# Kernel tuning notes

Measured on AMD Instinct MI355X. Metric: run time of the kernel, lower is better.

The kernel has to match this reference:

```python
import jax, jax.numpy as jnp
import numpy as np

N_NODES = 500_000
N_EDGES = 16_000_000
N_COLORS = 64


def _mix(v, c1, c2):
    """32-bit integer hash (lowbias32-style avalanche mix)."""
    v = v.astype(jnp.uint32)
    v = (v ^ (v >> 16)) * jnp.uint32(c1)
    v = (v ^ (v >> 13)) * jnp.uint32(c2)
    return v ^ (v >> 16)


def setup_inputs() -> dict:
    key = jax.random.key(0)
    k1, k2 = jax.random.split(key)
    x = jax.random.randint(k1, (N_NODES,), 0, N_COLORS, dtype=jnp.int32)
    edge_index = jax.random.randint(k2, (2, N_EDGES), 0, N_NODES, dtype=jnp.int32)
    return {"x": x, "edge_index": edge_index}


def reference(x, edge_index):
    """One Weisfeiler-Lehman color-refinement step.

    Faithful semantics of WLConvOptimized.forward: each node's new label is
    determined by the equivalence class of (own label, multiset of incoming
    neighbor labels). Instead of Python tuple-sort + hash()+dict, we use a
    permutation-invariant multiset hash (sum of two independent 32-bit hashes
    of neighbor labels, combined with the node's own label hash) and then a
    sort-based dense relabeling. Nodes get equal output labels iff their
    (label, neighbor-multiset) signatures collide -- same partition as the
    original (up to astronomically unlikely hash collisions); label numbering
    is canonical (sorted-signature order) rather than dict-insertion order.
    """
    num_nodes = x.shape[0]
    row, col = edge_index[0], edge_index[1]  # message flows row (src) -> col (dst)

    # two independent per-label hashes
    ha = _mix(x, 0x045D9F3B, 0x045D9F3B)
    hb = _mix(x, 0x9E3779B1, 0x85EBCA77)

    # permutation-invariant multiset hash of incoming neighbor labels (gather + scatter-add)
    sum_a = jnp.zeros(num_nodes, jnp.uint32).at[col].add(ha[row])
    sum_b = jnp.zeros(num_nodes, jnp.uint32).at[col].add(hb[row])

    # combine own label with neighbor multiset, re-avalanche
    sig_a = _mix(ha * jnp.uint32(0x27D4EB2F) + sum_a, 0xC2B2AE3D, 0x165667B1)
    sig_b = _mix(hb * jnp.uint32(0x61C88647) + sum_b, 0x045D9F3B, 0x27D4EB2F)

    # dense relabel: sort by (sig_a, sig_b), number distinct signatures 0..K-1
    order = jnp.lexsort((sig_b, sig_a))
    sa, sb = sig_a[order], sig_b[order]
    new_grp = jnp.concatenate([
        jnp.zeros(1, jnp.int32),
        ((sa[1:] != sa[:-1]) | (sb[1:] != sb[:-1])).astype(jnp.int32),
    ])
    labels_sorted = jnp.cumsum(new_grp).astype(jnp.int32)
    out = jnp.zeros(num_nodes, jnp.int32).at[order].set(labels_sorted)
    return out
```

## Files before the change

kernel.cpp:

```cpp
#include <hip/hip_runtime.h>
#include <stdint.h>

#define LOG_B 17
#define NB (1u << LOG_B)
#define FINE_NODES 1024
#define NBKT 512
#define CSH 10
#define EPB 16384

__host__ __device__ constexpr uint32_t cmix(uint32_t v, uint32_t c1, uint32_t c2) {
    v = (v ^ (v >> 16)) * c1;
    v = (v ^ (v >> 13)) * c2;
    return v ^ (v >> 16);
}

__device__ __forceinline__ uint32_t mixh(uint32_t v, uint32_t c1, uint32_t c2) {
    v = (v ^ (v >> 16)) * c1;
    v = (v ^ (v >> 13)) * c2;
    return v ^ (v >> 16);
}

struct Luts { uint32_t ha[64]; uint32_t hb[64]; };
constexpr Luts make_luts() {
    Luts l{};
    for (uint32_t i = 0; i < 64; i++) {
        l.ha[i] = cmix(i, 0x045D9F3Bu, 0x045D9F3Bu);
        l.hb[i] = cmix(i, 0x9E3779B1u, 0x85EBCA77u);
    }
    return l;
}
__constant__ Luts LUT = make_luts();

__global__ __launch_bounds__(256) void k_pre(const int4* __restrict__ x4,
                                             uchar4* __restrict__ xc4, int n4) {
    int i = blockIdx.x * 256 + threadIdx.x;
    if (i >= n4) return;
    int4 v = x4[i];
    xc4[i] = make_uchar4((uint8_t)v.x, (uint8_t)v.y, (uint8_t)v.z, (uint8_t)v.w);
}

__global__ __launch_bounds__(256) void k_bin(const int* __restrict__ row, const int* __restrict__ col,
                                             const uint8_t* __restrict__ xc, uint16_t* __restrict__ bins,
                                             uint32_t* __restrict__ cursor, int E, int cap) {
    __shared__ uint16_t stage[EPB];
    __shared__ uint32_t hist[NBKT];
    __shared__ uint16_t gb16[NBKT];
    __shared__ uint32_t wsum[4];
    int t = threadIdx.x;
    int lane = t & 63, wid = t >> 6;
    int base = blockIdx.x * EPB;
    int nend = min(E - base, EPB);
    for (int b = t; b < NBKT; b += 256) hist[b] = 0;
    __syncthreads();

    const int4* col4 = (const int4*)(col + base);
    const int4* row4 = (const int4*)(row + base);
    int n4 = nend >> 2;

    for (int k = t; k < n4; k += 256) {
        int4 c = col4[k];
        atomicAdd(&hist[(uint32_t)c.x >> CSH], 1u);
        atomicAdd(&hist[(uint32_t)c.y >> CSH], 1u);
        atomicAdd(&hist[(uint32_t)c.z >> CSH], 1u);
        atomicAdd(&hist[(uint32_t)c.w >> CSH], 1u);
    }
    for (int k = (n4 << 2) + t; k < nend; k += 256)
        atomicAdd(&hist[(uint32_t)col[base + k] >> CSH], 1u);
    __syncthreads();

    int b0 = 2 * t;
    uint32_t h0 = hist[b0], h1 = hist[b0 + 1];
    uint32_t s = h0 + h1;
    uint32_t inc = s;
    for (int off = 1; off < 64; off <<= 1) {
        uint32_t nv = __shfl_up(inc, (unsigned)off, 64);
        if (lane >= off) inc += nv;
    }
    if (lane == 63) wsum[wid] = inc;
    __syncthreads();
    uint32_t woff = 0;
    for (int w = 0; w < wid; w++) woff += wsum[w];
    uint32_t e0 = woff + inc - s;
    uint32_t g0 = h0 ? atomicAdd(&cursor[b0], h0) : 0u;
    uint32_t g1 = h1 ? atomicAdd(&cursor[b0 + 1], h1) : 0u;
    gb16[b0] = (uint16_t)g0;
    gb16[b0 + 1] = (uint16_t)g1;
    hist[b0] = e0 << 16;
    hist[b0 + 1] = (e0 + h0) << 16;
    __syncthreads();

    for (int k = t; k < n4; k += 256) {
        int4 c = col4[k];
        int4 r = row4[k];
        {
            uint32_t d = (uint32_t)c.x, b = d >> CSH;
            uint32_t o = atomicAdd(&hist[b], 1u);
            stage[(o >> 16) + (o & 0xFFFFu)] = (uint16_t)(((d & 1023u) << 6) | (uint32_t)xc[r.x]);
        }
        {
            uint32_t d = (uint32_t)c.y, b = d >> CSH;
            uint32_t o = atomicAdd(&hist[b], 1u);
            stage[(o >> 16) + (o & 0xFFFFu)] = (uint16_t)(((d & 1023u) << 6) | (uint32_t)xc[r.y]);
        }
        {
            uint32_t d = (uint32_t)c.z, b = d >> CSH;
            uint32_t o = atomicAdd(&hist[b], 1u);
            stage[(o >> 16) + (o & 0xFFFFu)] = (uint16_t)(((d & 1023u) << 6) | (uint32_t)xc[r.z]);
        }
        {
            uint32_t d = (uint32_t)c.w, b = d >> CSH;
            uint32_t o = atomicAdd(&hist[b], 1u);
            stage[(o >> 16) + (o & 0xFFFFu)] = (uint16_t)(((d & 1023u) << 6) | (uint32_t)xc[r.w]);
        }
    }
    for (int k = (n4 << 2) + t; k < nend; k += 256) {
        int i = base + k;
        uint32_t d = (uint32_t)col[i], b = d >> CSH;
        uint32_t o = atomicAdd(&hist[b], 1u);
        stage[(o >> 16) + (o & 0xFFFFu)] = (uint16_t)(((d & 1023u) << 6) | (uint32_t)xc[row[i]]);
    }
    __syncthreads();

    int sub = lane >> 4, l16 = lane & 15;
    for (int b = wid * 4 + sub; b < NBKT; b += 16) {
        uint32_t hv = hist[b];
        uint32_t cnt = hv & 0xFFFFu;
        if (!cnt) continue;
        uint32_t s0 = hv >> 16;
        uint16_t* dst = bins + (size_t)b * (uint32_t)cap + gb16[b];
        for (uint32_t off = l16; off < cnt; off += 16)
            dst[off] = stage[s0 + off];
    }
}

__global__ __launch_bounds__(512) void k_accsig(const uint16_t* __restrict__ bins,
                                                const uint32_t* __restrict__ cursor,
                                                const uint8_t* __restrict__ xc,
                                                unsigned long long* __restrict__ sigs,
                                                uint32_t* __restrict__ bcnt, int N, int cap) {
    __shared__ uint32_t cnt[FINE_NODES * 16];
    int t = threadIdx.x;
    int b = blockIdx.x;
    for (int i = t; i < FINE_NODES * 16; i += 512) cnt[i] = 0;
    __syncthreads();
    uint32_t m = cursor[b];
    const uint16_t* mybins = bins + (size_t)b * (uint32_t)cap;
    const uint2* p16v = (const uint2*)mybins;
    uint32_t m4 = m >> 2;
    for (uint32_t k = t; k < m4; k += 512) {
        uint2 rv = p16v[k];
        {
            uint32_t rec = rv.x & 0xFFFFu, n = rec >> 6, c = rec & 63u;
            atomicAdd(&cnt[n * 16 + (c >> 2)], 1u << (8u * (c & 3u)));
        }
        {
            uint32_t rec = rv.x >> 16, n = rec >> 6, c = rec & 63u;
            atomicAdd(&cnt[n * 16 + (c >> 2)], 1u << (8u * (c & 3u)));
        }
        {
            uint32_t rec = rv.y & 0xFFFFu, n = rec >> 6, c = rec & 63u;
            atomicAdd(&cnt[n * 16 + (c >> 2)], 1u << (8u * (c & 3u)));
        }
        {
            uint32_t rec = rv.y >> 16, n = rec >> 6, c = rec & 63u;
            atomicAdd(&cnt[n * 16 + (c >> 2)], 1u << (8u * (c & 3u)));
        }
    }
    for (uint32_t k = (m4 << 2) + t; k < m; k += 512) {
        uint32_t rec = mybins[k], n = rec >> 6, c = rec & 63u;
        atomicAdd(&cnt[n * 16 + (c >> 2)], 1u << (8u * (c & 3u)));
    }
    __syncthreads();

    for (int n = t; n < FINE_NODES; n += 512) {
        int g = b * FINE_NODES + n;
        if (g >= N) break;
        uint32_t sum_a = 0, sum_b = 0;
#pragma unroll
        for (int w = 0; w < 16; w++) {
            uint32_t wp = (uint32_t)(w + n) & 15u;
            uint32_t v = cnt[n * 16 + wp];
            uint32_t c0 = v & 255u, c1 = (v >> 8) & 255u, c2 = (v >> 16) & 255u, c3 = v >> 24;
            sum_a += c0 * LUT.ha[4 * wp] + c1 * LUT.ha[4 * wp + 1]
                   + c2 * LUT.ha[4 * wp + 2] + c3 * LUT.ha[4 * wp + 3];
            sum_b += c0 * LUT.hb[4 * wp] + c1 * LUT.hb[4 * wp + 1]
                   + c2 * LUT.hb[4 * wp + 2] + c3 * LUT.hb[4 * wp + 3];
        }
        uint32_t xv = (uint32_t)xc[g];
        uint32_t ha = LUT.ha[xv];
        uint32_t hb = LUT.hb[xv];
        uint32_t sa = mixh(ha * 0x27D4EB2Fu + sum_a, 0xC2B2AE3Du, 0x165667B1u);
        uint32_t sb = mixh(hb * 0x61C88647u + sum_b, 0x045D9F3Bu, 0x27D4EB2Fu);
        unsigned long long key = ((unsigned long long)sa << 32) | (unsigned long long)sb;
        sigs[g] = key;
        atomicAdd(&bcnt[(uint32_t)(key >> (64 - LOG_B))], 1u);
    }
}

__global__ __launch_bounds__(256) void k_scan1(const uint32_t* __restrict__ in,
                                               uint32_t* __restrict__ out,
                                               uint32_t* __restrict__ part) {
    __shared__ uint32_t wsum[4];
    int t = threadIdx.x;
    int lane = t & 63, wid = t >> 6;
    int base = blockIdx.x * 1024 + 4 * t;
    uint4 v = *(const uint4*)(in + base);
    uint32_t s = v.x + v.y + v.z + v.w;
    uint32_t inc = s;
    for (int off = 1; off < 64; off <<= 1) {
        uint32_t nv = __shfl_up(inc, (unsigned)off, 64);
        if (lane >= off) inc += nv;
    }
    if (lane == 63) wsum[wid] = inc;
    __syncthreads();
    uint32_t woff = 0;
    for (int w = 0; w < wid; w++) woff += wsum[w];
    uint32_t e = woff + inc - s;
    uint4 o;
    o.x = e; o.y = e + v.x; o.z = o.y + v.y; o.w = o.z + v.z;
    *(uint4*)(out + base) = o;
    if (t == 255) part[blockIdx.x] = wsum[0] + wsum[1] + wsum[2] + wsum[3];
}

__global__ void k_scan2(uint32_t* __restrict__ part) {
    __shared__ uint32_t s[256];
    int t = threadIdx.x;
    uint32_t v = part[t];
    s[t] = v;
    __syncthreads();
    for (int off = 1; off < 256; off <<= 1) {
        uint32_t add = (t >= off) ? s[t - off] : 0u;
        __syncthreads();
        s[t] += add;
        __syncthreads();
    }
    part[t] = s[t] - v;
}

__global__ __launch_bounds__(256) void k_scan3(uint32_t* __restrict__ out,
                                               const uint32_t* __restrict__ part) {
    int base = blockIdx.x * 1024 + 4 * threadIdx.x;
    uint32_t p = part[blockIdx.x];
    uint4 v = *(const uint4*)(out + base);
    v.x += p; v.y += p; v.z += p; v.w += p;
    *(uint4*)(out + base) = v;
}

__global__ void k_scatter(const unsigned long long* __restrict__ sigs,
                          const uint32_t* __restrict__ boff, uint32_t* __restrict__ bcur,
                          unsigned long long* __restrict__ skey, uint32_t* __restrict__ snode,
                          int N) {
    int i = blockIdx.x * blockDim.x + threadIdx.x;
    if (i >= N) return;
    unsigned long long key = sigs[i];
    uint32_t b = (uint32_t)(key >> (64 - LOG_B));
    uint32_t pos = boff[b] + atomicAdd(&bcur[b], 1u);
    skey[pos] = key;
    snode[pos] = (uint32_t)i;
}

__global__ void k_bsort(unsigned long long* __restrict__ skey, uint32_t* __restrict__ snode,
                        const uint32_t* __restrict__ boff, uint32_t* __restrict__ ldx,
                        uint32_t* __restrict__ dcnt, int N) {
    int b = blockIdx.x * blockDim.x + threadIdx.x;
    if (b >= (int)NB) return;
    uint32_t s0 = boff[b];
    uint32_t s1 = (b == (int)NB - 1) ? (uint32_t)N : boff[b + 1];
    for (uint32_t i = s0 + 1; i < s1; i++) {
        unsigned long long k = skey[i];
        uint32_t nd = snode[i];
        uint32_t j = i;
        while (j > s0 && skey[j - 1] > k) {
            skey[j] = skey[j - 1];
            snode[j] = snode[j - 1];
            j--;
        }
        skey[j] = k;
        snode[j] = nd;
    }
    uint32_t d = 0;
    unsigned long long prev = 0ull;
    for (uint32_t i = s0; i < s1; i++) {
        unsigned long long k = skey[i];
        if (i == s0 || k != prev) d++;
        prev = k;
        ldx[i] = d - 1;
    }
    dcnt[b] = d;
}

__global__ void k_out(const unsigned long long* __restrict__ skey,
                      const uint32_t* __restrict__ snode, const uint32_t* __restrict__ ldx,
                      const uint32_t* __restrict__ doff, int* __restrict__ out, int N) {
    int i = blockIdx.x * blockDim.x + threadIdx.x;
    if (i >= N) return;
    unsigned long long key = skey[i];
    uint32_t b = (uint32_t)(key >> (64 - LOG_B));
    out[snode[i]] = (int)(doff[b] + ldx[i]);
}

extern "C" void kernel_launch(void* const* d_in, const int* in_sizes, int n_in,
                              void* d_out, int out_size, void* d_ws, size_t ws_size,
                              hipStream_t stream) {
    const int* x = (const int*)d_in[0];
    const int* ei = (const int*)d_in[1];
    int N = in_sizes[0];
    int E = in_sizes[1] / 2;
    const int* row = ei;
    const int* col = ei + E;

    int nacc = (N + FINE_NODES - 1) / FINE_NODES;
    int cap = E / NBKT + (E / NBKT) / 16 + 1024;
    cap = (cap + 3) & ~3;

    char* p = (char*)d_ws;
    auto alloc = [&](size_t bytes) -> char* {
        char* r = p;
        p += (bytes + 255) & ~(size_t)255;
        return r;
    };
    uint32_t* cursor = (uint32_t*)alloc((size_t)NBKT * 4);
    uint32_t* bcnt   = (uint32_t*)alloc((size_t)NB * 4);
    uint32_t* bcur   = (uint32_t*)alloc((size_t)NB * 4);
    uint32_t* dcnt   = (uint32_t*)alloc((size_t)NB * 4);
    uint32_t* part   = (uint32_t*)alloc(256 * 4);
    size_t zbytes = (size_t)(p - (char*)d_ws);
    uint8_t* xc = (uint8_t*)alloc((size_t)N);
    unsigned long long* sigs = (unsigned long long*)alloc((size_t)N * 8);
    uint16_t* bins = (uint16_t*)alloc((size_t)NBKT * cap * 2);
    char* q = (char*)bins;
    auto alias = [&](size_t bytes) -> char* {
        char* r = q;
        q += (bytes + 255) & ~(size_t)255;
        return r;
    };
    unsigned long long* skey = (unsigned long long*)alias((size_t)N * 8);
    uint32_t* snode = (uint32_t*)alias((size_t)N * 4);
    uint32_t* ldx   = (uint32_t*)alias((size_t)N * 4);
    uint32_t* boff  = (uint32_t*)alias((size_t)NB * 4);
    uint32_t* doff  = (uint32_t*)alias((size_t)NB * 4);

    hipMemsetAsync(d_ws, 0, zbytes, stream);

    int nbN = (N + 255) / 256;
    int nbBin = (E + EPB - 1) / EPB;
    int n4 = N / 4;

    k_pre<<<(n4 + 255) / 256, 256, 0, stream>>>((const int4*)x, (uchar4*)xc, n4);
    k_bin<<<nbBin, 256, 0, stream>>>(row, col, xc, bins, cursor, E, cap);
    k_accsig<<<nacc, 512, 0, stream>>>(bins, cursor, xc, sigs, bcnt, N, cap);

    k_scan1<<<NB / 1024, 256, 0, stream>>>(bcnt, boff, part);
    k_scan2<<<1, 256, 0, stream>>>(part);
    k_scan3<<<NB / 1024, 256, 0, stream>>>(boff, part);

    k_scatter<<<nbN, 256, 0, stream>>>(sigs, boff, bcur, skey, snode, N);
    k_bsort<<<NB / 256, 256, 0, stream>>>(skey, snode, boff, ldx, dcnt, N);

    k_scan1<<<NB / 1024, 256, 0, stream>>>(dcnt, doff, part);
    k_scan2<<<1, 256, 0, stream>>>(part);
    k_scan3<<<NB / 1024, 256, 0, stream>>>(doff, part);

    k_out<<<nbN, 256, 0, stream>>>(skey, snode, ldx, doff, (int*)d_out, N);
}
```

Baseline: 434.8 us.

## Replace edge binning and shared-memory histograms with direct global atomic scatter-add

Removes the two-pass bucketed binning of edges and the per-bucket shared-memory color histogram. Each edge now gathers its source label, hashes it inline and does two global atomicAdds into per-node sumA/sumB arrays, followed by a per-node signature kernel. This drops the intermediate bins buffer and one pass over edges, but trades contention-free shared atomics for 32M random global atomics.

```diff
diff --git a/kernel.cpp b/kernel.cpp
--- a/kernel.cpp
+++ b/kernel.cpp
@@ -3,33 +3,12 @@
 
 #define LOG_B 17
 #define NB (1u << LOG_B)
-#define FINE_NODES 1024
-#define NBKT 512
-#define CSH 10
-#define EPB 16384
-
-__host__ __device__ constexpr uint32_t cmix(uint32_t v, uint32_t c1, uint32_t c2) {
-    v = (v ^ (v >> 16)) * c1;
-    v = (v ^ (v >> 13)) * c2;
-    return v ^ (v >> 16);
-}
 
 __device__ __forceinline__ uint32_t mixh(uint32_t v, uint32_t c1, uint32_t c2) {
     v = (v ^ (v >> 16)) * c1;
     v = (v ^ (v >> 13)) * c2;
     return v ^ (v >> 16);
 }
-
-struct Luts { uint32_t ha[64]; uint32_t hb[64]; };
-constexpr Luts make_luts() {
-    Luts l{};
-    for (uint32_t i = 0; i < 64; i++) {
-        l.ha[i] = cmix(i, 0x045D9F3Bu, 0x045D9F3Bu);
-        l.hb[i] = cmix(i, 0x9E3779B1u, 0x85EBCA77u);
-    }
-    return l;
-}
-__constant__ Luts LUT = make_luts();
 
 __global__ __launch_bounds__(256) void k_pre(const int4* __restrict__ x4,
                                              uchar4* __restrict__ xc4, int n4) {
@@ -39,162 +18,58 @@
     xc4[i] = make_uchar4((uint8_t)v.x, (uint8_t)v.y, (uint8_t)v.z, (uint8_t)v.w);
 }
 
-__global__ __launch_bounds__(256) void k_bin(const int* __restrict__ row, const int* __restrict__ col,
-                                             const uint8_t* __restrict__ xc, uint16_t* __restrict__ bins,
-                                             uint32_t* __restrict__ cursor, int E, int cap) {
-    __shared__ uint16_t stage[EPB];
-    __shared__ uint32_t hist[NBKT];
-    __shared__ uint16_t gb16[NBKT];
-    __shared__ uint32_t wsum[4];
-    int t = threadIdx.x;
-    int lane = t & 63, wid = t >> 6;
-    int base = blockIdx.x * EPB;
-    int nend = min(E - base, EPB);
-    for (int b = t; b < NBKT; b += 256) hist[b] = 0;
-    __syncthreads();
-
-    const int4* col4 = (const int4*)(col + base);
-    const int4* row4 = (const int4*)(row + base);
-    int n4 = nend >> 2;
-
-    for (int k = t; k < n4; k += 256) {
+__global__ __launch_bounds__(256) void k_edge(const int4* __restrict__ row4,
+                                              const int4* __restrict__ col4,
+                                              const int* __restrict__ row,
+                                              const int* __restrict__ col,
+                                              const uint8_t* __restrict__ xc,
+                                              uint32_t* __restrict__ sumA,
+                                              uint32_t* __restrict__ sumB,
+                                              int n4, int E) {
+    int stride = gridDim.x * 256;
+    for (int k = blockIdx.x * 256 + threadIdx.x; k < n4; k += stride) {
+        int4 r = row4[k];
         int4 c = col4[k];
-        atomicAdd(&hist[(uint32_t)c.x >> CSH], 1u);
-        atomicAdd(&hist[(uint32_t)c.y >> CSH], 1u);
-        atomicAdd(&hist[(uint32_t)c.z >> CSH], 1u);
-        atomicAdd(&hist[(uint32_t)c.w >> CSH], 1u);
-    }
-    for (int k = (n4 << 2) + t; k < nend; k += 256)
-        atomicAdd(&hist[(uint32_t)col[base + k] >> CSH], 1u);
-    __syncthreads();
-
-    int b0 = 2 * t;
-    uint32_t h0 = hist[b0], h1 = hist[b0 + 1];
-    uint32_t s = h0 + h1;
-    uint32_t inc = s;
-    for (int off = 1; off < 64; off <<= 1) {
-        uint32_t nv = __shfl_up(inc, (unsigned)off, 64);
-        if (lane >= off) inc += nv;
-    }
-    if (lane == 63) wsum[wid] = inc;
-    __syncthreads();
-    uint32_t woff = 0;
-    for (int w = 0; w < wid; w++) woff += wsum[w];
-    uint32_t e0 = woff + inc - s;
-    uint32_t g0 = h0 ? atomicAdd(&cursor[b0], h0) : 0u;
-    uint32_t g1 = h1 ? atomicAdd(&cursor[b0 + 1], h1) : 0u;
-    gb16[b0] = (uint16_t)g0;
-    gb16[b0 + 1] = (uint16_t)g1;
-    hist[b0] = e0 << 16;
-    hist[b0 + 1] = (e0 + h0) << 16;
-    __syncthreads();
-
-    for (int k = t; k < n4; k += 256) {
-        int4 c = col4[k];
-        int4 r = row4[k];
-        {
-            uint32_t d = (uint32_t)c.x, b = d >> CSH;
-            uint32_t o = atomicAdd(&hist[b], 1u);
-            stage[(o >> 16) + (o & 0xFFFFu)] = (uint16_t)(((d & 1023u) << 6) | (uint32_t)xc[r.x]);
-        }
-        {
-            uint32_t d = (uint32_t)c.y, b = d >> CSH;
-            uint32_t o = atomicAdd(&hist[b], 1u);
-            stage[(o >> 16) + (o & 0xFFFFu)] = (uint16_t)(((d & 1023u) << 6) | (uint32_t)xc[r.y]);
-        }
-        {
-            uint32_t d = (uint32_t)c.z, b = d >> CSH;
-            uint32_t o = atomicAdd(&hist[b], 1u);
-            stage[(o >> 16) + (o & 0xFFFFu)] = (uint16_t)(((d & 1023u) << 6) | (uint32_t)xc[r.z]);
-        }
-        {
-            uint32_t d = (uint32_t)c.w, b = d >> CSH;
-            uint32_t o = atomicAdd(&hist[b], 1u);
-            stage[(o >> 16) + (o & 0xFFFFu)] = (uint16_t)(((d & 1023u) << 6) | (uint32_t)xc[r.w]);
-        }
-    }
-    for (int k = (n4 << 2) + t; k < nend; k += 256) {
-        int i = base + k;
-        uint32_t d = (uint32_t)col[i], b = d >> CSH;
-        uint32_t o = atomicAdd(&hist[b], 1u);
-        stage[(o >> 16) + (o & 0xFFFFu)] = (uint16_t)(((d & 1023u) << 6) | (uint32_t)xc[row[i]]);
-    }
-    __syncthreads();
-
-    int sub = lane >> 4, l16 = lane & 15;
-    for (int b = wid * 4 + sub; b < NBKT; b += 16) {
-        uint32_t hv = hist[b];
-        uint32_t cnt = hv & 0xFFFFu;
-        if (!cnt) continue;
-        uint32_t s0 = hv >> 16;
-        uint16_t* dst = bins + (size_t)b * (uint32_t)cap + gb16[b];
-        for (uint32_t off = l16; off < cnt; off += 16)
-            dst[off] = stage[s0 + off];
-    }
-}
-
-__global__ __launch_bounds__(512) void k_accsig(const uint16_t* __restrict__ bins,
-                                                const uint32_t* __restrict__ cursor,
-                                                const uint8_t* __restrict__ xc,
-                                                unsigned long long* __restrict__ sigs,
-                                                uint32_t* __restrict__ bcnt, int N, int cap) {
-    __shared__ uint32_t cnt[FINE_NODES * 16];
-    int t = threadIdx.x;
-    int b = blockIdx.x;
-    for (int i = t; i < FINE_NODES * 16; i += 512) cnt[i] = 0;
-    __syncthreads();
-    uint32_t m = cursor[b];
-    const uint16_t* mybins = bins + (size_t)b * (uint32_t)cap;
-    const uint2* p16v = (const uint2*)mybins;
-    uint32_t m4 = m >> 2;
-    for (uint32_t k = t; k < m4; k += 512) {
-        uint2 rv = p16v[k];
-        {
-            uint32_t rec = rv.x & 0xFFFFu, n = rec >> 6, c = rec & 63u;
-            atomicAdd(&cnt[n * 16 + (c >> 2)], 1u << (8u * (c & 3u)));
-        }
-        {
-            uint32_t rec = rv.x >> 16, n = rec >> 6, c = rec & 63u;
-            atomicAdd(&cnt[n * 16 + (c >> 2)], 1u << (8u * (c & 3u)));
-        }
-        {
-            uint32_t rec = rv.y & 0xFFFFu, n = rec >> 6, c = rec & 63u;
-            atomicAdd(&cnt[n * 16 + (c >> 2)], 1u << (8u * (c & 3u)));
-        }
-        {
-            uint32_t rec = rv.y >> 16, n = rec >> 6, c = rec & 63u;
-            atomicAdd(&cnt[n * 16 + (c >> 2)], 1u << (8u * (c & 3u)));
-        }
-    }
-    for (uint32_t k = (m4 << 2) + t; k < m; k += 512) {
-        uint32_t rec = mybins[k], n = rec >> 6, c = rec & 63u;
-        atomicAdd(&cnt[n * 16 + (c >> 2)], 1u << (8u * (c & 3u)));
-    }
-    __syncthreads();
-
-    for (int n = t; n < FINE_NODES; n += 512) {
-        int g = b * FINE_NODES + n;
-        if (g >= N) break;
-        uint32_t sum_a = 0, sum_b = 0;
-#pragma unroll
-        for (int w = 0; w < 16; w++) {
-            uint32_t wp = (uint32_t)(w + n) & 15u;
-            uint32_t v = cnt[n * 16 + wp];
-            uint32_t c0 = v & 255u, c1 = (v >> 8) & 255u, c2 = (v >> 16) & 255u, c3 = v >> 24;
-            sum_a += c0 * LUT.ha[4 * wp] + c1 * LUT.ha[4 * wp + 1]
-                   + c2 * LUT.ha[4 * wp + 2] + c3 * LUT.ha[4 * wp + 3];
-            sum_b += c0 * LUT.hb[4 * wp] + c1 * LUT.hb[4 * wp + 1]
-                   + c2 * LUT.hb[4 * wp + 2] + c3 * LUT.hb[4 * wp + 3];
-        }
-        uint32_t xv = (uint32_t)xc[g];
-        uint32_t ha = LUT.ha[xv];
-        uint32_t hb = LUT.hb[xv];
-        uint32_t sa = mixh(ha * 0x27D4EB2Fu + sum_a, 0xC2B2AE3Du, 0x165667B1u);
-        uint32_t sb = mixh(hb * 0x61C88647u + sum_b, 0x045D9F3Bu, 0x27D4EB2Fu);
-        unsigned long long key = ((unsigned long long)sa << 32) | (unsigned long long)sb;
-        sigs[g] = key;
-        atomicAdd(&bcnt[(uint32_t)(key >> (64 - LOG_B))], 1u);
-    }
+        uint32_t l0 = xc[r.x], l1 = xc[r.y], l2 = xc[r.z], l3 = xc[r.w];
+        uint32_t a0 = mixh(l0, 0x045D9F3Bu, 0x045D9F3Bu);
+        uint32_t a1 = mixh(l1, 0x045D9F3Bu, 0x045D9F3Bu);
+        uint32_t a2 = mixh(l2, 0x045D9F3Bu, 0x045D9F3Bu);
+        uint32_t a3 = mixh(l3, 0x045D9F3Bu, 0x045D9F3Bu);
+        uint32_t b0 = mixh(l0, 0x9E3779B1u, 0x85EBCA77u);
+        uint32_t b1 = mixh(l1, 0x9E3779B1u, 0x85EBCA77u);
+        uint32_t b2 = mixh(l2, 0x9E3779B1u, 0x85EBCA77u);
+        uint32_t b3 = mixh(l3, 0x9E3779B1u, 0x85EBCA77u);
+        atomicAdd(&sumA[c.x], a0);
+        atomicAdd(&sumB[c.x], b0);
+        atomicAdd(&sumA[c.y], a1);
+        atomicAdd(&sumB[c.y], b1);
+        atomicAdd(&sumA[c.z], a2);
+        atomicAdd(&sumB[c.z], b2);
+        atomicAdd(&sumA[c.w], a3);
+        atomicAdd(&sumB[c.w], b3);
+    }
+    for (int i = (n4 << 2) + blockIdx.x * 256 + threadIdx.x; i < E; i += stride) {
+        uint32_t l = xc[row[i]];
+        atomicAdd(&sumA[col[i]], mixh(l, 0x045D9F3Bu, 0x045D9F3Bu));
+        atomicAdd(&sumB[col[i]], mixh(l, 0x9E3779B1u, 0x85EBCA77u));
+    }
+}
+
+__global__ __launch_bounds__(256) void k_sig(const uint32_t* __restrict__ sumA,
+                                             const uint32_t* __restrict__ sumB,
+                                             const uint8_t* __restrict__ xc,
+                                             unsigned long long* __restrict__ sigs,
+                                             uint32_t* __restrict__ bcnt, int N) {
+    int i = blockIdx.x * 256 + threadIdx.x;
+    if (i >= N) return;
+    uint32_t xv = (uint32_t)xc[i];
+    uint32_t ha = mixh(xv, 0x045D9F3Bu, 0x045D9F3Bu);
+    uint32_t hb = mixh(xv, 0x9E3779B1u, 0x85EBCA77u);
+    uint32_t sa = mixh(ha * 0x27D4EB2Fu + sumA[i], 0xC2B2AE3Du, 0x165667B1u);
+    uint32_t sb = mixh(hb * 0x61C88647u + sumB[i], 0x045D9F3Bu, 0x27D4EB2Fu);
+    unsigned long long key = ((unsigned long long)sa << 32) | (unsigned long long)sb;
+    sigs[i] = key;
+    atomicAdd(&bcnt[(uint32_t)(key >> (64 - LOG_B))], 1u);
 }
 
 __global__ __launch_bounds__(256) void k_scan1(const uint32_t* __restrict__ in,
@@ -309,46 +184,39 @@
     const int* row = ei;
     const int* col = ei + E;
 
-    int nacc = (N + FINE_NODES - 1) / FINE_NODES;
-    int cap = E / NBKT + (E / NBKT) / 16 + 1024;
-    cap = (cap + 3) & ~3;
-
     char* p = (char*)d_ws;
     auto alloc = [&](size_t bytes) -> char* {
         char* r = p;
         p += (bytes + 255) & ~(size_t)255;
         return r;
     };
-    uint32_t* cursor = (uint32_t*)alloc((size_t)NBKT * 4);
-    uint32_t* bcnt   = (uint32_t*)alloc((size_t)NB * 4);
-    uint32_t* bcur   = (uint32_t*)alloc((size_t)NB * 4);
-    uint32_t* dcnt   = (uint32_t*)alloc((size_t)NB * 4);
-    uint32_t* part   = (uint32_t*)alloc(256 * 4);
+    uint32_t* sumA = (uint32_t*)alloc((size_t)N * 4);
+    uint32_t* sumB = (uint32_t*)alloc((size_t)N * 4);
+    uint32_t* bcnt = (uint32_t*)alloc((size_t)NB * 4);
+    uint32_t* bcur = (uint32_t*)alloc((size_t)NB * 4);
+    uint32_t* dcnt = (uint32_t*)alloc((size_t)NB * 4);
+    uint32_t* part = (uint32_t*)alloc(256 * 4);
     size_t zbytes = (size_t)(p - (char*)d_ws);
     uint8_t* xc = (uint8_t*)alloc((size_t)N);
     unsigned long long* sigs = (unsigned long long*)alloc((size_t)N * 8);
-    uint16_t* bins = (uint16_t*)alloc((size_t)NBKT * cap * 2);
-    char* q = (char*)bins;
-    auto alias = [&](size_t bytes) -> char* {
-        char* r = q;
-        q += (bytes + 255) & ~(size_t)255;
-        return r;
-    };
-    unsigned long long* skey = (unsigned long long*)alias((size_t)N * 8);
-    uint32_t* snode = (uint32_t*)alias((size_t)N * 4);
-    uint32_t* ldx   = (uint32_t*)alias((size_t)N * 4);
-    uint32_t* boff  = (uint32_t*)alias((size_t)NB * 4);
-    uint32_t* doff  = (uint32_t*)alias((size_t)NB * 4);
+    unsigned long long* skey = (unsigned long long*)alloc((size_t)N * 8);
+    uint32_t* snode = (uint32_t*)alloc((size_t)N * 4);
+    uint32_t* ldx   = (uint32_t*)alloc((size_t)N * 4);
+    uint32_t* boff  = (uint32_t*)alloc((size_t)NB * 4);
+    uint32_t* doff  = (uint32_t*)alloc((size_t)NB * 4);
 
     hipMemsetAsync(d_ws, 0, zbytes, stream);
 
     int nbN = (N + 255) / 256;
-    int nbBin = (E + EPB - 1) / EPB;
-    int n4 = N / 4;
-
-    k_pre<<<(n4 + 255) / 256, 256, 0, stream>>>((const int4*)x, (uchar4*)xc, n4);
-    k_bin<<<nbBin, 256, 0, stream>>>(row, col, xc, bins, cursor, E, cap);
-    k_accsig<<<nacc, 512, 0, stream>>>(bins, cursor, xc, sigs, bcnt, N, cap);
+    int n4N = N / 4;
+    int n4E = E / 4;
+    int nbE = (n4E + 255) / 256;
+    if (nbE > 2048) nbE = 2048;
+
+    k_pre<<<(n4N + 255) / 256, 256, 0, stream>>>((const int4*)x, (uchar4*)xc, n4N);
+    k_edge<<<nbE, 256, 0, stream>>>((const int4*)row, (const int4*)col, row, col,
+                                    xc, sumA, sumB, n4E, E);
+    k_sig<<<nbN, 256, 0, stream>>>(sumA, sumB, xc, sigs, bcnt, N);
 
     k_scan1<<<NB / 1024, 256, 0, stream>>>(bcnt, boff, part);
     k_scan2<<<1, 256, 0, stream>>>(part);
```

After: 1.455 ms. 235% more time.
